# Kernel optimization log

Measured on AMD Instinct MI355X. Metric: run time of the kernel, lower is better.

Reference implementation:

```python
import jax, jax.numpy as jnp
import numpy as np

TEMPERATURE = 8.0  # sqrt(d_k) with d_k = 64
MASK_FILL = -65504.0  # fp16 min, as in the original


def setup_inputs() -> dict:
    key = jax.random.key(0)
    kq, kk, kv, km = jax.random.split(key, 4)
    BH, L, D = 16, 2048, 64
    q = jax.random.normal(kq, (BH, L, D), dtype=jnp.float32)
    k = jax.random.normal(kk, (BH, L, D), dtype=jnp.float32)
    v = jax.random.normal(kv, (BH, L, D), dtype=jnp.float32)
    mask = jax.random.randint(km, (BH, L, L), 0, 2).astype(jnp.bool_)
    return {"q": q, "k": k, "v": v, "mask": mask}


def reference(q, k, v, mask):
    # attn = q @ k^T / temperature, masked_fill, softmax over last dim
    attn = jnp.einsum("bqd,bkd->bqk", q, k) / TEMPERATURE
    attn = jnp.where(mask, MASK_FILL, attn)
    attn = jax.nn.softmax(attn, axis=2)
    # dropout with p=0.0 is identity (eval-mode reference)
    output = jnp.einsum("bqk,bkd->bqd", attn, v)
    return (output, attn)
```

## Files before the change

### kernel.cpp

```cpp
#include <hip/hip_runtime.h>

#define BH 16
#define L 2048
#define D 64
#define QB 32
#define KB 64
#define NKT (L / KB)
#define SCALE 0.125f
#define MASK_FILL -65504.0f

typedef __bf16 bf16x8 __attribute__((ext_vector_type(8)));
typedef float f32x4 __attribute__((ext_vector_type(4)));

__device__ __forceinline__ unsigned f2bf(float f) {
    union { float f; unsigned u; } x; x.f = f;
    return (x.u + 0x7FFFu + ((x.u >> 16) & 1u)) >> 16;
}
__device__ __forceinline__ float bf2f(unsigned short h) {
    union { unsigned u; float f; } x; x.u = ((unsigned)h) << 16;
    return x.f;
}


extern "C" __global__ __launch_bounds__(256)
void preK(const float* __restrict__ k, uint4* __restrict__ wsK)
{
    int idx = blockIdx.x * 256 + threadIdx.x;
    int c   = idx & 7;
    int key = (idx >> 3) & (L - 1);
    int bh  = idx >> 14;
    const float4* src = (const float4*)(k + ((size_t)(bh * L + key) * D + c * 8));
    float4 a = src[0], b = src[1];
    uint4 o;
    o.x = f2bf(a.x) | (f2bf(a.y) << 16);
    o.y = f2bf(a.z) | (f2bf(a.w) << 16);
    o.z = f2bf(b.x) | (f2bf(b.y) << 16);
    o.w = f2bf(b.z) | (f2bf(b.w) << 16);
    wsK[(size_t)(bh * L + key) * 8 + (c ^ (key & 7))] = o;
}

extern "C" __global__ __launch_bounds__(256)
void preV(const float* __restrict__ v, uint4* __restrict__ wsVt)
{
    __shared__ float sT[64 * 68];
    int b = blockIdx.x;
    int bh = b >> 5, kt = b & 31;
    const float4* src = (const float4*)(v + ((size_t)bh * L + kt * 64) * D);
    int t = threadIdx.x;
    #pragma unroll
    for (int i = 0; i < 4; ++i) {
        int i4 = i * 256 + t;
        int key = i4 >> 4, c4 = i4 & 15;
        float4 val = src[i4];
        *(float4*)&sT[key * 68 + c4 * 4] = val;
    }
    __syncthreads();
    int d = t >> 2, cg = t & 3;
    #pragma unroll
    for (int j = 0; j < 2; ++j) {
        int c = cg + j * 4;
        unsigned pk[4];
        #pragma unroll
        for (int e = 0; e < 4; ++e) {
            float x0 = sT[(c * 8 + e * 2    ) * 68 + d];
            float x1 = sT[(c * 8 + e * 2 + 1) * 68 + d];
            pk[e] = f2bf(x0) | (f2bf(x1) << 16);
        }
        wsVt[((size_t)(bh * 32 + kt) * 64 + d) * 8 + (c ^ (d & 7))] =
            make_uint4(pk[0], pk[1], pk[2], pk[3]);
    }
}


extern "C" __global__ __launch_bounds__(256, 4)
void sdpa_main(const float* __restrict__ q, const uint4* __restrict__ gKall,
               const uint4* __restrict__ gVall, const int* __restrict__ mask,
               float* __restrict__ out, float* __restrict__ attn)
{
    __shared__ unsigned short sP[2][QB * 72];
    __shared__ float sPart[4][16];

    const int tid = threadIdx.x, lane = tid & 63, w = tid >> 6;
    const int wr = w & 1, wn = w >> 1;
    const int quad = lane >> 4, l15 = lane & 15;
    const int p = blockIdx.x, bh = p & 15, qb = p >> 4, q0 = qb * QB;

    const uint4* gK = gKall + (size_t)bh * L * 8;
    const uint4* gV = gVall + (size_t)bh * L * 8;

    const float* Qp = q + (size_t)(bh * L + q0 + wr * 16 + l15) * D + quad * 8;
    float4 qv0 = *(const float4*)(Qp);
    float4 qv1 = *(const float4*)(Qp + 4);
    float4 qv2 = *(const float4*)(Qp + 32);
    float4 qv3 = *(const float4*)(Qp + 36);
    union { bf16x8 v; unsigned short s[8]; } qa0u, qa1u;
    qa0u.s[0] = f2bf(qv0.x); qa0u.s[1] = f2bf(qv0.y); qa0u.s[2] = f2bf(qv0.z); qa0u.s[3] = f2bf(qv0.w);
    qa0u.s[4] = f2bf(qv1.x); qa0u.s[5] = f2bf(qv1.y); qa0u.s[6] = f2bf(qv1.z); qa0u.s[7] = f2bf(qv1.w);
    qa1u.s[0] = f2bf(qv2.x); qa1u.s[1] = f2bf(qv2.y); qa1u.s[2] = f2bf(qv2.z); qa1u.s[3] = f2bf(qv2.w);
    qa1u.s[4] = f2bf(qv3.x); qa1u.s[5] = f2bf(qv3.y); qa1u.s[6] = f2bf(qv3.z); qa1u.s[7] = f2bf(qv3.w);
    const bf16x8 qa0 = qa0u.v, qa1 = qa1u.v;

    const int key0 = wn * 32 + l15;
    const int key1 = key0 + 16;
    const int s7 = l15 & 7;
    const int o00 = key0 * 8 + ((quad    ) ^ s7);
    const int o01 = key0 * 8 + ((quad + 4) ^ s7);
    const int o10 = key1 * 8 + ((quad    ) ^ s7);
    const int o11 = key1 * 8 + ((quad + 4) ^ s7);

    auto loadK = [&](int kt, bf16x8& a, bf16x8& b, bf16x8& c, bf16x8& d) {
        const uint4* base = gK + (size_t)kt * 512;
        a = *(const bf16x8*)(base + o00);
        b = *(const bf16x8*)(base + o01);
        c = *(const bf16x8*)(base + o10);
        d = *(const bf16x8*)(base + o11);
    };
    auto loadV = [&](int kt, bf16x8& a, bf16x8& b, bf16x8& c, bf16x8& d) {
        const uint4* base = gV + (size_t)kt * 512;
        a = *(const bf16x8*)(base + o00);
        b = *(const bf16x8*)(base + o01);
        c = *(const bf16x8*)(base + o10);
        d = *(const bf16x8*)(base + o11);
    };

    const int* Mb0 = mask + ((size_t)bh * L + q0 + wr * 16 + quad * 4) * L
                          + wn * 32 + l15;

    unsigned mb[8] = {0u, 0u, 0u, 0u, 0u, 0u, 0u, 0u};

    float lsum[4] = {0.f, 0.f, 0.f, 0.f};

    bf16x8 k0c, k1c, k2c, k3c;
    loadK(0, k0c, k1c, k2c, k3c);
    int mc[8];
    #pragma unroll
    for (int r = 0; r < 4; ++r) {
        mc[2 * r]     = Mb0[(size_t)r * L];
        mc[2 * r + 1] = Mb0[(size_t)r * L + 16];
    }

    for (int kt = 0; kt < NKT; ++kt) {
        bf16x8 k0n, k1n, k2n, k3n;
        int mn[8];
        const bool pf = (kt + 1 < NKT);
        if (pf) {
            loadK(kt + 1, k0n, k1n, k2n, k3n);
            const int* mrow = Mb0 + (kt + 1) * 64;
            #pragma unroll
            for (int r = 0; r < 4; ++r) {
                mn[2 * r]     = mrow[(size_t)r * L];
                mn[2 * r + 1] = mrow[(size_t)r * L + 16];
            }
        }
        f32x4 acc[2];
        acc[0] = (f32x4){0.f, 0.f, 0.f, 0.f};
        acc[0] = __builtin_amdgcn_mfma_f32_16x16x32_bf16(qa0, k0c, acc[0], 0, 0, 0);
        acc[0] = __builtin_amdgcn_mfma_f32_16x16x32_bf16(qa1, k1c, acc[0], 0, 0, 0);
        acc[1] = (f32x4){0.f, 0.f, 0.f, 0.f};
        acc[1] = __builtin_amdgcn_mfma_f32_16x16x32_bf16(qa0, k2c, acc[1], 0, 0, 0);
        acc[1] = __builtin_amdgcn_mfma_f32_16x16x32_bf16(qa1, k3c, acc[1], 0, 0, 0);
        #pragma unroll
        for (int j = 0; j < 2; ++j) {
            #pragma unroll
            for (int r = 0; r < 4; ++r) {
                float val = acc[j][r] * SCALE;
                const bool m = (mc[2 * r + j] != 0);
                mb[2 * r + j] |= (m ? (1u << kt) : 0u);
                val = m ? MASK_FILL : val;
                lsum[r] += __expf(val);
            }
        }
        if (pf) {
            k0c = k0n; k1c = k1n; k2c = k2n; k3c = k3n;
            #pragma unroll
            for (int i = 0; i < 8; ++i) mc[i] = mn[i];
        }
    }

    #pragma unroll
    for (int off = 1; off < 16; off <<= 1)
        #pragma unroll
        for (int r = 0; r < 4; ++r) lsum[r] += __shfl_xor(lsum[r], off, 64);
    if (l15 == 0) {
        #pragma unroll
        for (int r = 0; r < 4; ++r) sPart[w][quad * 4 + r] = lsum[r];
    }
    __syncthreads();
    float rinv[4];
    #pragma unroll
    for (int r = 0; r < 4; ++r)
        rinv[r] = 1.0f / (sPart[wr][quad * 4 + r] + sPart[wr + 2][quad * 4 + r]);

    f32x4 oacc[2];
    oacc[0] = (f32x4){0.f, 0.f, 0.f, 0.f};
    oacc[1] = (f32x4){0.f, 0.f, 0.f, 0.f};
    float* Ab = attn + ((size_t)bh * L + q0) * L;

    loadK(0, k0c, k1c, k2c, k3c);
    for (int kt = 0; kt < NKT; ++kt) {
        f32x4 acc[2];
        acc[0] = (f32x4){0.f, 0.f, 0.f, 0.f};
        acc[0] = __builtin_amdgcn_mfma_f32_16x16x32_bf16(qa0, k0c, acc[0], 0, 0, 0);
        acc[0] = __builtin_amdgcn_mfma_f32_16x16x32_bf16(qa1, k1c, acc[0], 0, 0, 0);
        acc[1] = (f32x4){0.f, 0.f, 0.f, 0.f};
        acc[1] = __builtin_amdgcn_mfma_f32_16x16x32_bf16(qa0, k2c, acc[1], 0, 0, 0);
        acc[1] = __builtin_amdgcn_mfma_f32_16x16x32_bf16(qa1, k3c, acc[1], 0, 0, 0);

        unsigned short* sPb = sP[kt & 1];
        #pragma unroll
        for (int j = 0; j < 2; ++j) {
            const int col = key0 + j * 16;
            #pragma unroll
            for (int r = 0; r < 4; ++r) {
                float val = acc[j][r] * SCALE;
                val = ((mb[2 * r + j] >> kt) & 1u) ? MASK_FILL : val;
                float pr = __expf(val) * rinv[r];
                const int row = wr * 16 + quad * 4 + r;
                Ab[(size_t)row * L + kt * 64 + col] = pr;
                sPb[row * 72 + col] = (unsigned short)f2bf(pr);
            }
        }
        __syncthreads();
        if (kt + 1 < NKT) loadK(kt + 1, k0c, k1c, k2c, k3c);

        const bf16x8 pa0 = *(const bf16x8*)&sPb[(wr * 16 + l15) * 72 + quad * 8];
        const bf16x8 pa1 = *(const bf16x8*)&sPb[(wr * 16 + l15) * 72 + quad * 8 + 32];
        bf16x8 v0, v1, v2, v3;
        loadV(kt, v0, v1, v2, v3);
        oacc[0] = __builtin_amdgcn_mfma_f32_16x16x32_bf16(pa0, v0, oacc[0], 0, 0, 0);
        oacc[0] = __builtin_amdgcn_mfma_f32_16x16x32_bf16(pa1, v1, oacc[0], 0, 0, 0);
        oacc[1] = __builtin_amdgcn_mfma_f32_16x16x32_bf16(pa0, v2, oacc[1], 0, 0, 0);
        oacc[1] = __builtin_amdgcn_mfma_f32_16x16x32_bf16(pa1, v3, oacc[1], 0, 0, 0);
    }

    float* Ob = out + ((size_t)bh * L + q0) * D;
    #pragma unroll
    for (int j = 0; j < 2; ++j)
        #pragma unroll
        for (int r = 0; r < 4; ++r)
            Ob[(size_t)(wr * 16 + quad * 4 + r) * D + (wn * 2 + j) * 16 + l15] = oacc[j][r];
}


extern "C" __global__ __launch_bounds__(256, 2)
void sdpa_kernel(const float* __restrict__ q, const float* __restrict__ k,
                 const float* __restrict__ v, const int* __restrict__ mask,
                 float* __restrict__ out, float* __restrict__ attn)
{
    __shared__ unsigned short fQ[64 * 72];
    __shared__ unsigned short fK[64 * 72];
    __shared__ unsigned short fVt[64 * 72];
    __shared__ unsigned short fP[64 * 72];
    __shared__ unsigned long long fM[64 * 33];

    const int tid  = threadIdx.x;
    const int lane = tid & 63;
    const int w    = tid >> 6;
    const int quad = lane >> 4;
    const int l15  = lane & 15;

    const int p  = blockIdx.x;
    const int bh = p & (BH - 1);
    const int qb = p >> 4;
    const int q0 = qb * 64;

    const size_t base = (size_t)bh * L * D;
    const float* Qb = q + base + (size_t)q0 * D;
    const float* Kb = k + base;
    const float* Vb = v + base;
    const int*   Mb = mask + (size_t)bh * L * L + (size_t)q0 * L;
    float*       Ab = attn + (size_t)bh * L * L + (size_t)q0 * L;
    float*       Ob = out  + base + (size_t)q0 * D;

    {
        const float2* Qs = (const float2*)Qb;
        for (int i = 0; i < 8; ++i) {
            int idx = i * 256 + tid;
            int row = idx >> 5, d2 = idx & 31;
            float2 val = Qs[idx];
            unsigned pk = f2bf(val.x) | (f2bf(val.y) << 16);
            *(unsigned*)&fQ[row * 72 + d2 * 2] = pk;
        }
    }
    for (int rr = 0; rr < 16; ++rr) {
        int row = w * 16 + rr;
        const int4* Ms = (const int4*)(Mb + (size_t)row * L);
        for (int it = 0; it < 8; ++it) {
            int4 mv = Ms[it * 64 + lane];
            unsigned long long b0 = __ballot(mv.x != 0);
            unsigned long long b1 = __ballot(mv.y != 0);
            unsigned long long b2 = __ballot(mv.z != 0);
            unsigned long long b3 = __ballot(mv.w != 0);
            if (lane == 0) {
                unsigned long long* dst = &fM[row * 33 + it * 4];
                dst[0] = b0; dst[1] = b1; dst[2] = b2; dst[3] = b3;
            }
        }
    }
    __syncthreads();

    const int qrow = w * 16 + l15;
    bf16x8 qa0 = *(const bf16x8*)&fQ[qrow * 72 + quad * 8];
    bf16x8 qa1 = *(const bf16x8*)&fQ[qrow * 72 + quad * 8 + 32];

    float lsum[4] = {0.f, 0.f, 0.f, 0.f};
    for (int kt = 0; kt < 32; ++kt) {
        const int k0 = kt * 64;
        __syncthreads();
        {
            const float2* Ks = (const float2*)(Kb + (size_t)k0 * D);
            for (int i = 0; i < 8; ++i) {
                int idx = i * 256 + tid;
                int row = idx >> 5, d2 = idx & 31;
                float2 val = Ks[idx];
                unsigned pk = f2bf(val.x) | (f2bf(val.y) << 16);
                *(unsigned*)&fK[row * 72 + d2 * 2] = pk;
            }
        }
        __syncthreads();
        f32x4 acc[4];
        for (int nt = 0; nt < 4; ++nt) {
            bf16x8 b0 = *(const bf16x8*)&fK[(nt * 16 + l15) * 72 + quad * 8];
            bf16x8 b1 = *(const bf16x8*)&fK[(nt * 16 + l15) * 72 + quad * 8 + 32];
            f32x4 c = {0.f, 0.f, 0.f, 0.f};
            c = __builtin_amdgcn_mfma_f32_16x16x32_bf16(qa0, b0, c, 0, 0, 0);
            c = __builtin_amdgcn_mfma_f32_16x16x32_bf16(qa1, b1, c, 0, 0, 0);
            acc[nt] = c;
        }
        const int widx = (k0 >> 8) * 4 + (lane & 3);
        const int bsh0 = (k0 >> 2) + (l15 >> 2);
        for (int r = 0; r < 4; ++r) {
            int row = w * 16 + quad * 4 + r;
            unsigned long long mwv = fM[row * 33 + widx];
            float s = 0.f;
            for (int nt = 0; nt < 4; ++nt) {
                float val = acc[nt][r] * SCALE;
                int bit = (int)((mwv >> ((bsh0 + nt * 4) & 63)) & 1ull);
                val = bit ? MASK_FILL : val;
                s += __expf(val);
            }
            lsum[r] += s;
        }
    }
    for (int off = 1; off < 16; off <<= 1)
        for (int r = 0; r < 4; ++r) lsum[r] += __shfl_xor(lsum[r], off, 64);
    float rinv[4];
    for (int r = 0; r < 4; ++r) rinv[r] = 1.0f / lsum[r];

    f32x4 oacc[4];
    for (int nt = 0; nt < 4; ++nt) oacc[nt] = (f32x4){0.f, 0.f, 0.f, 0.f};

    for (int kt = 0; kt < 32; ++kt) {
        const int k0 = kt * 64;
        __syncthreads();
        {
            const float2* Ks = (const float2*)(Kb + (size_t)k0 * D);
            for (int i = 0; i < 8; ++i) {
                int idx = i * 256 + tid;
                int row = idx >> 5, d2 = idx & 31;
                float2 val = Ks[idx];
                unsigned pk = f2bf(val.x) | (f2bf(val.y) << 16);
                *(unsigned*)&fK[row * 72 + d2 * 2] = pk;
            }
        }
        {
            unsigned pk[8];
            for (int jj = 0; jj < 16; ++jj) {
                float val = Vb[(size_t)(k0 + w * 16 + jj) * D + lane];
                unsigned bv = f2bf(val);
                if (jj & 1) pk[jj >> 1] |= bv << 16;
                else        pk[jj >> 1]  = bv;
            }
            uint4* dst = (uint4*)&fVt[lane * 72 + w * 16];
            dst[0] = make_uint4(pk[0], pk[1], pk[2], pk[3]);
            dst[1] = make_uint4(pk[4], pk[5], pk[6], pk[7]);
        }
        __syncthreads();
        f32x4 acc[4];
        for (int nt = 0; nt < 4; ++nt) {
            bf16x8 b0 = *(const bf16x8*)&fK[(nt * 16 + l15) * 72 + quad * 8];
            bf16x8 b1 = *(const bf16x8*)&fK[(nt * 16 + l15) * 72 + quad * 8 + 32];
            f32x4 c = {0.f, 0.f, 0.f, 0.f};
            c = __builtin_amdgcn_mfma_f32_16x16x32_bf16(qa0, b0, c, 0, 0, 0);
            c = __builtin_amdgcn_mfma_f32_16x16x32_bf16(qa1, b1, c, 0, 0, 0);
            acc[nt] = c;
        }
        const int widx = (k0 >> 8) * 4 + (lane & 3);
        const int bsh0 = (k0 >> 2) + (l15 >> 2);
        for (int r = 0; r < 4; ++r) {
            int row = w * 16 + quad * 4 + r;
            unsigned long long mwv = fM[row * 33 + widx];
            for (int nt = 0; nt < 4; ++nt) {
                float val = acc[nt][r] * SCALE;
                int bit = (int)((mwv >> ((bsh0 + nt * 4) & 63)) & 1ull);
                val = bit ? MASK_FILL : val;
                float pr = __expf(val) * rinv[r];
                fP[row * 72 + nt * 16 + l15] = (unsigned short)f2bf(pr);
            }
        }
        for (int it = 0; it < 4; ++it) {
            int row = w * 16 + it * 4 + quad;
            unsigned long long pv = *(const unsigned long long*)&fP[row * 72 + l15 * 4];
            float4 o;
            o.x = bf2f((unsigned short)(pv         & 0xFFFF));
            o.y = bf2f((unsigned short)((pv >> 16) & 0xFFFF));
            o.z = bf2f((unsigned short)((pv >> 32) & 0xFFFF));
            o.w = bf2f((unsigned short)((pv >> 48) & 0xFFFF));
            *(float4*)&Ab[(size_t)row * L + k0 + l15 * 4] = o;
        }
        {
            bf16x8 pa0 = *(const bf16x8*)&fP[qrow * 72 + quad * 8];
            bf16x8 pa1 = *(const bf16x8*)&fP[qrow * 72 + quad * 8 + 32];
            for (int nt = 0; nt < 4; ++nt) {
                bf16x8 vb0 = *(const bf16x8*)&fVt[(nt * 16 + l15) * 72 + quad * 8];
                bf16x8 vb1 = *(const bf16x8*)&fVt[(nt * 16 + l15) * 72 + quad * 8 + 32];
                oacc[nt] = __builtin_amdgcn_mfma_f32_16x16x32_bf16(pa0, vb0, oacc[nt], 0, 0, 0);
                oacc[nt] = __builtin_amdgcn_mfma_f32_16x16x32_bf16(pa1, vb1, oacc[nt], 0, 0, 0);
            }
        }
    }
    for (int nt = 0; nt < 4; ++nt)
        for (int r = 0; r < 4; ++r)
            Ob[(size_t)(w * 16 + quad * 4 + r) * D + nt * 16 + l15] = oacc[nt][r];
}


extern "C" void kernel_launch(void* const* d_in, const int* in_sizes, int n_in,
                              void* d_out, int out_size, void* d_ws, size_t ws_size,
                              hipStream_t stream)
{
    const float* q    = (const float*)d_in[0];
    const float* k    = (const float*)d_in[1];
    const float* v    = (const float*)d_in[2];
    const int*   mask = (const int*)d_in[3];
    float* out  = (float*)d_out;
    float* attn = out + (size_t)BH * L * D;

    const size_t WS_K  = 0;
    const size_t WS_VT = (size_t)BH * L * D * 2;
    const size_t NEED  = WS_VT + (size_t)BH * L * D * 2;

    if (ws_size >= NEED) {
        uint4* wsK  = (uint4*)((char*)d_ws + WS_K);
        uint4* wsVt = (uint4*)((char*)d_ws + WS_VT);
        hipLaunchKernelGGL(preK, dim3(1024), dim3(256), 0, stream, k, wsK);
        hipLaunchKernelGGL(preV, dim3(512),  dim3(256), 0, stream, v, wsVt);
        hipLaunchKernelGGL(sdpa_main, dim3(BH * (L / QB)), dim3(256), 0, stream,
                           q, (const uint4*)wsK, (const uint4*)wsVt, mask, out, attn);
    } else {
        hipLaunchKernelGGL(sdpa_kernel, dim3(BH * (L / 64)), dim3(256), 0, stream,
                           q, k, v, mask, out, attn);
    }
}
```

Measured before the change: 605.7 us.

## Pre-pack mask into bitwords and double-buffer K loads in softmax-sum pass

Adds a preM kernel that converts the int32 mask into 64-bit ballot bitmasks, one word per 64 keys, so the main kernel reads 8 bytes per row-tile instead of scattered 4-byte ints. The first pass is unrolled by two with two K register buffers for deeper prefetch. Masked entries are zeroed after the exp rather than by substituting the fill value. The second pass issues the V load earlier and replaces __syncthreads with an explicit lgkmcnt wait plus barrier. The extra kernel still reads the full mask once, and the workspace grows to hold the bitmask.

```diff
diff --git a/kernel.cpp b/kernel.cpp
--- a/kernel.cpp
+++ b/kernel.cpp
@@ -71,10 +71,32 @@
     }
 }
 
+extern "C" __global__ __launch_bounds__(256)
+void preM(const int* __restrict__ mask, unsigned long long* __restrict__ wsM)
+{
+    __shared__ unsigned long long sW[16 * 32];
+    int b = blockIdx.x;
+    size_t row0 = (size_t)b * 16;
+    int w = threadIdx.x >> 6, lane = threadIdx.x & 63;
+    const int* src = mask + row0 * L;
+    for (int rr = 0; rr < 4; ++rr) {
+        int r = w * 4 + rr;
+        #pragma unroll 8
+        for (int wd = 0; wd < 32; ++wd) {
+            int val = src[(size_t)r * L + wd * 64 + lane];
+            unsigned long long bal = __ballot(val != 0);
+            if (lane == 0) sW[r * 32 + wd] = bal;
+        }
+    }
+    __syncthreads();
+    int t = threadIdx.x;
+    ((uint4*)wsM)[(size_t)b * 256 + t] = ((const uint4*)sW)[t];
+}
+
 
 extern "C" __global__ __launch_bounds__(256, 4)
 void sdpa_main(const float* __restrict__ q, const uint4* __restrict__ gKall,
-               const uint4* __restrict__ gVall, const int* __restrict__ mask,
+               const uint4* __restrict__ gVall, const unsigned long long* __restrict__ wsM,
                float* __restrict__ out, float* __restrict__ attn)
 {
     __shared__ unsigned short sP[2][QB * 72];
@@ -123,57 +145,62 @@
         d = *(const bf16x8*)(base + o11);
     };
 
-    const int* Mb0 = mask + ((size_t)bh * L + q0 + wr * 16 + quad * 4) * L
-                          + wn * 32 + l15;
+    const unsigned long long* Mw = wsM + (size_t)(bh * L + q0 + wr * 16 + quad * 4) * 32;
 
     unsigned mb[8] = {0u, 0u, 0u, 0u, 0u, 0u, 0u, 0u};
 
     float lsum[4] = {0.f, 0.f, 0.f, 0.f};
 
-    bf16x8 k0c, k1c, k2c, k3c;
-    loadK(0, k0c, k1c, k2c, k3c);
-    int mc[8];
-    #pragma unroll
-    for (int r = 0; r < 4; ++r) {
-        mc[2 * r]     = Mb0[(size_t)r * L];
-        mc[2 * r + 1] = Mb0[(size_t)r * L + 16];
-    }
-
-    for (int kt = 0; kt < NKT; ++kt) {
-        bf16x8 k0n, k1n, k2n, k3n;
-        int mn[8];
-        const bool pf = (kt + 1 < NKT);
-        if (pf) {
-            loadK(kt + 1, k0n, k1n, k2n, k3n);
-            const int* mrow = Mb0 + (kt + 1) * 64;
+    bf16x8 kA0, kA1, kA2, kA3, kB0, kB1, kB2, kB3;
+    loadK(0, kA0, kA1, kA2, kA3);
+    loadK(1, kB0, kB1, kB2, kB3);
+
+    for (int kt = 0; kt < NKT; kt += 2) {
+        unsigned long long mw0[4], mw1[4];
+        #pragma unroll
+        for (int r = 0; r < 4; ++r) {
+            mw0[r] = Mw[r * 32 + kt];
+            mw1[r] = Mw[r * 32 + kt + 1];
+        }
+        {
+            f32x4 acc0 = (f32x4){0.f, 0.f, 0.f, 0.f};
+            f32x4 acc1 = (f32x4){0.f, 0.f, 0.f, 0.f};
+            acc0 = __builtin_amdgcn_mfma_f32_16x16x32_bf16(qa0, kA0, acc0, 0, 0, 0);
+            acc0 = __builtin_amdgcn_mfma_f32_16x16x32_bf16(qa1, kA1, acc0, 0, 0, 0);
+            acc1 = __builtin_amdgcn_mfma_f32_16x16x32_bf16(qa0, kA2, acc1, 0, 0, 0);
+            acc1 = __builtin_amdgcn_mfma_f32_16x16x32_bf16(qa1, kA3, acc1, 0, 0, 0);
+            if (kt + 2 < NKT) loadK(kt + 2, kA0, kA1, kA2, kA3);
             #pragma unroll
-            for (int r = 0; r < 4; ++r) {
-                mn[2 * r]     = mrow[(size_t)r * L];
-                mn[2 * r + 1] = mrow[(size_t)r * L + 16];
-            }
-        }
-        f32x4 acc[2];
-        acc[0] = (f32x4){0.f, 0.f, 0.f, 0.f};
-        acc[0] = __builtin_amdgcn_mfma_f32_16x16x32_bf16(qa0, k0c, acc[0], 0, 0, 0);
-        acc[0] = __builtin_amdgcn_mfma_f32_16x16x32_bf16(qa1, k1c, acc[0], 0, 0, 0);
-        acc[1] = (f32x4){0.f, 0.f, 0.f, 0.f};
-        acc[1] = __builtin_amdgcn_mfma_f32_16x16x32_bf16(qa0, k2c, acc[1], 0, 0, 0);
-        acc[1] = __builtin_amdgcn_mfma_f32_16x16x32_bf16(qa1, k3c, acc[1], 0, 0, 0);
-        #pragma unroll
-        for (int j = 0; j < 2; ++j) {
+            for (int j = 0; j < 2; ++j) {
+                const int sh = key0 + j * 16;
+                #pragma unroll
+                for (int r = 0; r < 4; ++r) {
+                    unsigned bit = (unsigned)((mw0[r] >> sh) & 1ull);
+                    mb[2 * r + j] |= bit << kt;
+                    float e = __expf((j ? acc1[r] : acc0[r]) * SCALE);
+                    lsum[r] += bit ? 0.f : e;
+                }
+            }
+        }
+        {
+            f32x4 acc0 = (f32x4){0.f, 0.f, 0.f, 0.f};
+            f32x4 acc1 = (f32x4){0.f, 0.f, 0.f, 0.f};
+            acc0 = __builtin_amdgcn_mfma_f32_16x16x32_bf16(qa0, kB0, acc0, 0, 0, 0);
+            acc0 = __builtin_amdgcn_mfma_f32_16x16x32_bf16(qa1, kB1, acc0, 0, 0, 0);
+            acc1 = __builtin_amdgcn_mfma_f32_16x16x32_bf16(qa0, kB2, acc1, 0, 0, 0);
+            acc1 = __builtin_amdgcn_mfma_f32_16x16x32_bf16(qa1, kB3, acc1, 0, 0, 0);
+            if (kt + 3 < NKT) loadK(kt + 3, kB0, kB1, kB2, kB3);
             #pragma unroll
-            for (int r = 0; r < 4; ++r) {
-                float val = acc[j][r] * SCALE;
-                const bool m = (mc[2 * r + j] != 0);
-                mb[2 * r + j] |= (m ? (1u << kt) : 0u);
-                val = m ? MASK_FILL : val;
-                lsum[r] += __expf(val);
-            }
-        }
-        if (pf) {
-            k0c = k0n; k1c = k1n; k2c = k2n; k3c = k3n;
-            #pragma unroll
-            for (int i = 0; i < 8; ++i) mc[i] = mn[i];
+            for (int j = 0; j < 2; ++j) {
+                const int sh = key0 + j * 16;
+                #pragma unroll
+                for (int r = 0; r < 4; ++r) {
+                    unsigned bit = (unsigned)((mw1[r] >> sh) & 1ull);
+                    mb[2 * r + j] |= bit << (kt + 1);
+                    float e = __expf((j ? acc1[r] : acc0[r]) * SCALE);
+                    lsum[r] += bit ? 0.f : e;
+                }
+            }
         }
     }
 
@@ -196,15 +223,18 @@
     oacc[1] = (f32x4){0.f, 0.f, 0.f, 0.f};
     float* Ab = attn + ((size_t)bh * L + q0) * L;
 
+    bf16x8 k0c, k1c, k2c, k3c;
     loadK(0, k0c, k1c, k2c, k3c);
     for (int kt = 0; kt < NKT; ++kt) {
-        f32x4 acc[2];
-        acc[0] = (f32x4){0.f, 0.f, 0.f, 0.f};
-        acc[0] = __builtin_amdgcn_mfma_f32_16x16x32_bf16(qa0, k0c, acc[0], 0, 0, 0);
-        acc[0] = __builtin_amdgcn_mfma_f32_16x16x32_bf16(qa1, k1c, acc[0], 0, 0, 0);
-        acc[1] = (f32x4){0.f, 0.f, 0.f, 0.f};
-        acc[1] = __builtin_amdgcn_mfma_f32_16x16x32_bf16(qa0, k2c, acc[1], 0, 0, 0);
-        acc[1] = __builtin_amdgcn_mfma_f32_16x16x32_bf16(qa1, k3c, acc[1], 0, 0, 0);
+        bf16x8 v0, v1, v2, v3;
+        loadV(kt, v0, v1, v2, v3);
+
+        f32x4 acc0 = (f32x4){0.f, 0.f, 0.f, 0.f};
+        f32x4 acc1 = (f32x4){0.f, 0.f, 0.f, 0.f};
+        acc0 = __builtin_amdgcn_mfma_f32_16x16x32_bf16(qa0, k0c, acc0, 0, 0, 0);
+        acc0 = __builtin_amdgcn_mfma_f32_16x16x32_bf16(qa1, k1c, acc0, 0, 0, 0);
+        acc1 = __builtin_amdgcn_mfma_f32_16x16x32_bf16(qa0, k2c, acc1, 0, 0, 0);
+        acc1 = __builtin_amdgcn_mfma_f32_16x16x32_bf16(qa1, k3c, acc1, 0, 0, 0);
 
         unsigned short* sPb = sP[kt & 1];
         #pragma unroll
@@ -212,21 +242,19 @@
             const int col = key0 + j * 16;
             #pragma unroll
             for (int r = 0; r < 4; ++r) {
-                float val = acc[j][r] * SCALE;
-                val = ((mb[2 * r + j] >> kt) & 1u) ? MASK_FILL : val;
-                float pr = __expf(val) * rinv[r];
+                float e = __expf((j ? acc1[r] : acc0[r]) * SCALE);
+                float pr = (((mb[2 * r + j] >> kt) & 1u) ? 0.f : e) * rinv[r];
                 const int row = wr * 16 + quad * 4 + r;
                 Ab[(size_t)row * L + kt * 64 + col] = pr;
                 sPb[row * 72 + col] = (unsigned short)f2bf(pr);
             }
         }
-        __syncthreads();
+        asm volatile("s_waitcnt lgkmcnt(0)\n\ts_barrier" ::: "memory");
+
         if (kt + 1 < NKT) loadK(kt + 1, k0c, k1c, k2c, k3c);
 
         const bf16x8 pa0 = *(const bf16x8*)&sPb[(wr * 16 + l15) * 72 + quad * 8];
         const bf16x8 pa1 = *(const bf16x8*)&sPb[(wr * 16 + l15) * 72 + quad * 8 + 32];
-        bf16x8 v0, v1, v2, v3;
-        loadV(kt, v0, v1, v2, v3);
         oacc[0] = __builtin_amdgcn_mfma_f32_16x16x32_bf16(pa0, v0, oacc[0], 0, 0, 0);
         oacc[0] = __builtin_amdgcn_mfma_f32_16x16x32_bf16(pa1, v1, oacc[0], 0, 0, 0);
         oacc[1] = __builtin_amdgcn_mfma_f32_16x16x32_bf16(pa0, v2, oacc[1], 0, 0, 0);
@@ -438,15 +466,18 @@
 
     const size_t WS_K  = 0;
     const size_t WS_VT = (size_t)BH * L * D * 2;
-    const size_t NEED  = WS_VT + (size_t)BH * L * D * 2;
+    const size_t WS_M  = WS_VT + (size_t)BH * L * D * 2;
+    const size_t NEED  = WS_M + (size_t)BH * L * 32 * 8;
 
     if (ws_size >= NEED) {
         uint4* wsK  = (uint4*)((char*)d_ws + WS_K);
         uint4* wsVt = (uint4*)((char*)d_ws + WS_VT);
+        unsigned long long* wsM = (unsigned long long*)((char*)d_ws + WS_M);
         hipLaunchKernelGGL(preK, dim3(1024), dim3(256), 0, stream, k, wsK);
         hipLaunchKernelGGL(preV, dim3(512),  dim3(256), 0, stream, v, wsVt);
+        hipLaunchKernelGGL(preM, dim3(2048), dim3(256), 0, stream, mask, wsM);
         hipLaunchKernelGGL(sdpa_main, dim3(BH * (L / QB)), dim3(256), 0, stream,
-                           q, (const uint4*)wsK, (const uint4*)wsVt, mask, out, attn);
+                           q, (const uint4*)wsK, (const uint4*)wsVt, wsM, out, attn);
     } else {
         hipLaunchKernelGGL(sdpa_kernel, dim3(BH * (L / 64)), dim3(256), 0, stream,
                            q, k, v, mask, out, attn);
```

After: 600.5 us. No clear change (-0.9%).
